# Kernel tuning notes

Hardware: AMD Instinct MI355X
Metric: run time of the kernel (lower is better)

Reference implementation:

```python
import jax, jax.numpy as jnp
import numpy as np

TOPK = 32

def softsign(x):
    return x / (1.0 + jnp.abs(x))

def setup_inputs() -> dict:
    key = jax.random.key(0)
    k1, k2, k3 = jax.random.split(key, 3)
    B, Q, S, D = 1, 4096, 32768, 256
    return {
        "query_val": jax.random.normal(k1, (B, Q, D), dtype=jnp.float32),
        "source_val": jax.random.normal(k2, (B, S, D), dtype=jnp.float32),
        "source_state": jax.random.normal(k3, (B, S), dtype=jnp.float32),
    }

def reference(query_val, source_val, source_state):
    # pairwise scores (dot-product similarity): [B, Q, S]
    scores = jnp.einsum("bqd,bsd->bqs", query_val, source_val)
    # global top-k over sources == streaming blockwise top-k merge in the original
    top_scores, top_idx = jax.lax.top_k(scores, TOPK)  # [B, Q, K]
    edges = softsign(top_scores)                        # edge_compress_fn
    # gather_state_by_indices: [B, Q, K]
    sel_state = jnp.take_along_axis(source_state[:, None, :], top_idx, axis=-1)
    # gather_val_by_indices: [B, Q, K, D]
    sel_val = jnp.take_along_axis(source_val[:, None, :, :], top_idx[..., None], axis=2)
    delta_state = jnp.sum(edges * sel_state, axis=-1)          # [B, Q]
    delta_val = jnp.sum(edges[..., None] * sel_val, axis=-2)   # [B, Q, D]
    return delta_state, delta_val
```

## Files before the change

kernel.cpp:

```cpp
#include <hip/hip_runtime.h>
#include <stdint.h>

typedef unsigned int u32;
typedef unsigned long long u64;
typedef unsigned short u16;
typedef unsigned char u8;

#define NQ 4096
#define NS 32768
#define ND 256
#define TOPK 32
#define CAP 256
#define CAP2 24
#define ZT 2.75f

#define QB 256
#define SB 32
#define NSLICE 32
#define SLICE (NS / NSLICE)
#define CH (SLICE / SB)

typedef __attribute__((ext_vector_type(8))) __bf16 bf16x8;
typedef __attribute__((ext_vector_type(4))) float f32x4;

#define QB_OFF   (NS * ND * 2)
#define TQ_OFF   (QB_OFF + NQ * ND * 2)
#define C8_OFF   (TQ_OFF + NQ * 4)
#define CD_OFF   (C8_OFF + NQ * NSLICE)

__device__ __forceinline__ u16 f2bf(float x) {
  u32 u = __float_as_uint(x);
  u32 r = u + 0x7FFFu + ((u >> 16) & 1u);
  return (u16)(r >> 16);
}

__global__ void k_prep_src(const float* __restrict__ src, uint4* __restrict__ dst) {
  int t = blockIdx.x * 256 + threadIdx.x;
  const float4* s4 = (const float4*)src + (size_t)t * 2;
  float4 a = s4[0], b = s4[1];
  uint4 o;
  o.x = (u32)f2bf(a.x) | ((u32)f2bf(a.y) << 16);
  o.y = (u32)f2bf(a.z) | ((u32)f2bf(a.w) << 16);
  o.z = (u32)f2bf(b.x) | ((u32)f2bf(b.y) << 16);
  o.w = (u32)f2bf(b.z) | ((u32)f2bf(b.w) << 16);
  dst[t] = o;
}

__global__ void k_prep_q(const float* __restrict__ qv, u16* __restrict__ qb,
                         float* __restrict__ tq) {
  int lane = threadIdx.x & 63, w = threadIdx.x >> 6;
  int q = blockIdx.x * 4 + w;
  float4 v = *((const float4*)(qv + (size_t)q * ND) + lane);
  uint2 p;
  p.x = (u32)f2bf(v.x) | ((u32)f2bf(v.y) << 16);
  p.y = (u32)f2bf(v.z) | ((u32)f2bf(v.w) << 16);
  *((uint2*)(qb + (size_t)q * ND) + lane) = p;
  float s = v.x * v.x + v.y * v.y + v.z * v.z + v.w * v.w;
  #pragma unroll
  for (int o = 1; o < 64; o <<= 1) s += __shfl_xor(s, o, 64);
  if (lane == 0) tq[q] = ZT * sqrtf(s);
}

__global__ __launch_bounds__(256, 2) void k_screen(
    const u16* __restrict__ qb, const u16* __restrict__ srcb,
    const float* __restrict__ tq, u8* __restrict__ cnt8, u32* __restrict__ cand2) {
  __shared__ __align__(16) u16 lds[2][SB * ND];
  __shared__ u32 bcnt[QB];
  const int tid  = threadIdx.x;
  const int lane = tid & 63;
  const int w    = tid >> 6;
  const int l15  = lane & 15, lhi = lane >> 4;

  const int id   = blockIdx.x;
  const int xcd  = id & 7;
  const int rank = id >> 3;
  const int by   = xcd * 4 + (rank >> 4);
  const int bx   = rank & 15;

  const int qbase = bx * QB + w * 64;
  const int sbase = by * SLICE;

  bcnt[tid] = 0u;

  bf16x8 afrag[4][8];
  float  thr[4][4];
  #pragma unroll
  for (int mt = 0; mt < 4; ++mt) {
    const u16* qp = qb + (size_t)(qbase + mt * 16 + l15) * ND;
    #pragma unroll
    for (int ks = 0; ks < 8; ++ks)
      afrag[mt][ks] = *((const bf16x8*)(qp + ks * 32 + lhi * 8));
    #pragma unroll
    for (int r = 0; r < 4; ++r) thr[mt][r] = tq[qbase + mt * 16 + lhi * 4 + r];
  }

  int goff[4];
  #pragma unroll
  for (int i = 0; i < 4; ++i) {
    int slot = i * 256 + tid;
    int row  = slot >> 5;
    int o    = (slot & 31) ^ (row & 7);
    goff[i]  = row * ND + o * 8;
  }

#define STAGE(b, c)                                                              \
  {                                                                              \
    const u16* sp_ = srcb + (size_t)(sbase + (c) * SB) * ND;                     \
    _Pragma("unroll")                                                            \
    for (int i_ = 0; i_ < 4; ++i_)                                               \
      __builtin_amdgcn_global_load_lds(                                          \
          (const __attribute__((address_space(1))) void*)(sp_ + goff[i_]),       \
          (__attribute__((address_space(3))) void*)(&lds[b][(i_ * 256 + tid) * 8]), \
          16, 0, 0);                                                             \
  }

#define COMPUTE(b, srow0)                                                        \
  {                                                                              \
    f32x4 acc[4][2];                                                             \
    _Pragma("unroll")                                                            \
    for (int mt = 0; mt < 4; ++mt)                                               \
      _Pragma("unroll")                                                          \
      for (int nt = 0; nt < 2; ++nt) acc[mt][nt] = (f32x4){0.f, 0.f, 0.f, 0.f};  \
    _Pragma("unroll")                                                            \
    for (int ks = 0; ks < 8; ++ks) {                                             \
      bf16x8 bfr[2];                                                             \
      _Pragma("unroll")                                                          \
      for (int nt = 0; nt < 2; ++nt) {                                           \
        int r_ = nt * 16 + l15;                                                  \
        int o_ = ks * 4 + lhi;                                                   \
        int slot_ = r_ * 32 + (o_ ^ (r_ & 7));                                   \
        bfr[nt] = *((const bf16x8*)(&lds[b][slot_ * 8]));                        \
      }                                                                          \
      _Pragma("unroll")                                                          \
      for (int mt = 0; mt < 4; ++mt)                                             \
        _Pragma("unroll")                                                        \
        for (int nt = 0; nt < 2; ++nt)                                           \
          acc[mt][nt] = __builtin_amdgcn_mfma_f32_16x16x32_bf16(                 \
              afrag[mt][ks], bfr[nt], acc[mt][nt], 0, 0, 0);                     \
    }                                                                            \
    _Pragma("unroll")                                                            \
    for (int mt = 0; mt < 4; ++mt)                                               \
      _Pragma("unroll")                                                          \
      for (int nt = 0; nt < 2; ++nt)                                             \
        _Pragma("unroll")                                                        \
        for (int r_ = 0; r_ < 4; ++r_) {                                         \
          float sc_ = acc[mt][nt][r_];                                           \
          if (sc_ > thr[mt][r_]) {                                               \
            int ql_ = w * 64 + mt * 16 + lhi * 4 + r_;                           \
            u32 off_ = atomicAdd(&bcnt[ql_], 1u);                                \
            if (off_ < CAP2)                                                     \
              cand2[(((size_t)(qbase + mt * 16 + lhi * 4 + r_)) * NSLICE + by) * CAP2 + off_] = \
                  ((u32)((srow0) + nt * 16 + l15) << 16) | (u32)f2bf(sc_);       \
          }                                                                      \
        }                                                                        \
  }

  STAGE(0, 0);
  __syncthreads();
  int cur = 0;
  for (int c = 0; c < CH - 1; ++c) {
    STAGE(cur ^ 1, c + 1);
    COMPUTE(cur, sbase + c * SB);
    __syncthreads();
    cur ^= 1;
  }
  COMPUTE(cur, sbase + (CH - 1) * SB);
#undef STAGE
#undef COMPUTE

  __syncthreads();
  {
    u32 c = bcnt[tid];
    cnt8[(size_t)by * NQ + bx * QB + tid] = (u8)(c < CAP2 ? c : CAP2);
  }
}

__global__ __launch_bounds__(256) void k_finish(
    const float* __restrict__ qval, const float* __restrict__ sval,
    const float* __restrict__ sstate, const u8* __restrict__ cnt8,
    const u32* __restrict__ cand2, float* __restrict__ out) {
  const int q = blockIdx.x;
  const int tid = threadIdx.x;
  const int lane = tid & 63, w = tid >> 6;
  __shared__ u16  scnt[NSLICE];
  __shared__ u16  soff[NSLICE];
  __shared__ u32  skey[CAP];
  __shared__ u32  sidxl[CAP];
  __shared__ float sexact[64];
  __shared__ u32  ssrc[64];
  __shared__ float fw[TOPK];
  __shared__ u32  fi[TOPK];

  if (tid < NSLICE) scnt[tid] = cnt8[(size_t)tid * NQ + q];
  skey[tid] = 0u;
  __syncthreads();
  if (tid == 0) {
    u32 a = 0;
    #pragma unroll
    for (int s = 0; s < NSLICE; ++s) { soff[s] = (u16)a; a += scnt[s]; }
  }
  __syncthreads();

  {
    int s = tid >> 3, j0 = tid & 7;
    #pragma unroll
    for (int rep = 0; rep < 3; ++rep) {
      int j = j0 + rep * 8;
      if (j < (int)scnt[s]) {
        int p = (int)soff[s] + j;
        if (p < CAP) {
          u32 ent = cand2[((size_t)q * NSLICE + s) * CAP2 + j];
          skey[p]  = ((ent & 0xFFFFu) << 8) | (u32)p;
          sidxl[p] = ent >> 16;
        }
      }
    }
  }
  __syncthreads();

  {
    u32 key = skey[tid];
    #pragma unroll
    for (int k = 2; k <= 256; k <<= 1) {
      #pragma unroll
      for (int j = k >> 1; j > 0; j >>= 1) {
        u32 o;
        if (j >= 64) {
          skey[tid] = key;
          __syncthreads();
          o = skey[tid ^ j];
          __syncthreads();
        } else {
          o = __shfl_xor(key, j, 64);
        }
        bool keepMax = ((tid & j) == 0) == ((tid & k) == 0);
        key = keepMax ? (key > o ? key : o) : (key > o ? o : key);
      }
    }
    skey[tid] = key;
  }
  __syncthreads();

  const int l16 = lane & 15, sub = lane >> 4;
  float4 qf[4];
  #pragma unroll
  for (int j = 0; j < 4; ++j)
    qf[j] = *((const float4*)(qval + (size_t)q * ND) + l16 * 4 + j);
  #pragma unroll
  for (int p = 0; p < 4; ++p) {
    int e = w * 16 + p * 4 + sub;
    u32 key = skey[e];
    u32 si = sidxl[key & 0xFFu];
    float dp = 0.f;
    if (key) {
      const float4* vp = (const float4*)(sval + (size_t)si * ND) + l16 * 4;
      #pragma unroll
      for (int j = 0; j < 4; ++j) {
        float4 v = vp[j];
        dp += qf[j].x * v.x + qf[j].y * v.y + qf[j].z * v.z + qf[j].w * v.w;
      }
    }
    #pragma unroll
    for (int o = 1; o < 16; o <<= 1) dp += __shfl_xor(dp, o, 64);
    if (l16 == 0) { sexact[e] = key ? dp : -3.0e38f; ssrc[e] = si; }
  }
  __syncthreads();

  if (w == 0) {
    float sc = sexact[lane];
    u32 si  = ssrc[lane];
    u32 kb  = __float_as_uint(sc);
    kb = kb ^ (u32)(((int)kb >> 31) | 0x80000000);
    u64 kk = ((u64)kb << 32) | (u32)(~si);
    #pragma unroll
    for (int k = 2; k <= 64; k <<= 1) {
      #pragma unroll
      for (int j = k >> 1; j > 0; j >>= 1) {
        u64 o = __shfl_xor(kk, j, 64);
        bool keepMax = (((lane & j) == 0) == ((lane & k) == 0));
        kk = keepMax ? (kk > o ? kk : o) : (kk > o ? o : kk);
      }
    }
    u32 si2 = ~((u32)kk);
    u32 kb2 = (u32)(kk >> 32);
    u32 fb  = (kb2 & 0x80000000u) ? (kb2 ^ 0x80000000u) : ~kb2;
    float s = __uint_as_float(fb);
    bool ok = (lane < TOPK) && (s > -1.0e38f);
    float edge = ok ? (s / (1.f + fabsf(s))) : 0.f;
    float contrib = ok ? edge * sstate[si2] : 0.f;
    if (lane < TOPK) { fw[lane] = edge; fi[lane] = ok ? si2 : 0u; }
    #pragma unroll
    for (int o = 1; o < 64; o <<= 1) contrib += __shfl_xor(contrib, o, 64);
    if (lane == 0) out[q] = contrib;
  }
  __syncthreads();

  float acc = 0.f;
  #pragma unroll 8
  for (int k = 0; k < TOPK; ++k)
    acc += fw[k] * sval[(size_t)fi[k] * ND + tid];
  out[NQ + (size_t)q * ND + tid] = acc;
}

extern "C" void kernel_launch(void* const* d_in, const int* in_sizes, int n_in,
                              void* d_out, int out_size, void* d_ws, size_t ws_size,
                              hipStream_t stream) {
  const float* qval   = (const float*)d_in[0];
  const float* sval   = (const float*)d_in[1];
  const float* sstate = (const float*)d_in[2];
  float* out = (float*)d_out;
  char*  ws  = (char*)d_ws;
  u16*   srcb  = (u16*)ws;
  u16*   qbuf  = (u16*)(ws + QB_OFF);
  float* tq    = (float*)(ws + TQ_OFF);
  u8*    cnt8  = (u8*)(ws + C8_OFF);
  u32*   cand2 = (u32*)(ws + CD_OFF);

  k_prep_src<<<(NS * ND / 8) / 256, 256, 0, stream>>>(sval, (uint4*)srcb);
  k_prep_q<<<NQ / 4, 256, 0, stream>>>(qval, qbuf, tq);
  k_screen<<<(NQ / QB) * NSLICE, 256, 0, stream>>>(qbuf, srcb, tq, cnt8, cand2);
  k_finish<<<NQ, 256, 0, stream>>>(qval, sval, sstate, cnt8, cand2, out);
}
```

Measured before the change: 151.7 us.

## Merge prep kernels, double-chunk screen pipeline, rescore only 48 candidates

Merges the two bf16 prep kernels into one launch so a kernel boundary disappears. The screen kernel now stages two source chunks per iteration into a 4-buffer LDS ring and computes both before one barrier, halving the barrier count at the cost of twice the LDS (64 KB), which may limit occupancy at 2 blocks/CU. The finish kernel rescores only the top 48 approximate candidates instead of 64, cutting fp32 gathers but raising the risk of missing a true top-32 entry when bf16 screening misorders scores.

```diff
diff --git a/kernel.cpp b/kernel.cpp
--- a/kernel.cpp
+++ b/kernel.cpp
@@ -34,37 +34,39 @@
   return (u16)(r >> 16);
 }
 
-__global__ void k_prep_src(const float* __restrict__ src, uint4* __restrict__ dst) {
-  int t = blockIdx.x * 256 + threadIdx.x;
-  const float4* s4 = (const float4*)src + (size_t)t * 2;
-  float4 a = s4[0], b = s4[1];
-  uint4 o;
-  o.x = (u32)f2bf(a.x) | ((u32)f2bf(a.y) << 16);
-  o.y = (u32)f2bf(a.z) | ((u32)f2bf(a.w) << 16);
-  o.z = (u32)f2bf(b.x) | ((u32)f2bf(b.y) << 16);
-  o.w = (u32)f2bf(b.z) | ((u32)f2bf(b.w) << 16);
-  dst[t] = o;
-}
-
-__global__ void k_prep_q(const float* __restrict__ qv, u16* __restrict__ qb,
-                         float* __restrict__ tq) {
-  int lane = threadIdx.x & 63, w = threadIdx.x >> 6;
-  int q = blockIdx.x * 4 + w;
-  float4 v = *((const float4*)(qv + (size_t)q * ND) + lane);
-  uint2 p;
-  p.x = (u32)f2bf(v.x) | ((u32)f2bf(v.y) << 16);
-  p.y = (u32)f2bf(v.z) | ((u32)f2bf(v.w) << 16);
-  *((uint2*)(qb + (size_t)q * ND) + lane) = p;
-  float s = v.x * v.x + v.y * v.y + v.z * v.z + v.w * v.w;
-  #pragma unroll
-  for (int o = 1; o < 64; o <<= 1) s += __shfl_xor(s, o, 64);
-  if (lane == 0) tq[q] = ZT * sqrtf(s);
+__global__ void k_prep(const float* __restrict__ src, uint4* __restrict__ dst,
+                       const float* __restrict__ qv, u16* __restrict__ qb,
+                       float* __restrict__ tq) {
+  const int b = blockIdx.x;
+  if (b < (NS * ND / 8) / 256) {
+    int t = b * 256 + threadIdx.x;
+    const float4* s4 = (const float4*)src + (size_t)t * 2;
+    float4 a = s4[0], c = s4[1];
+    uint4 o;
+    o.x = (u32)f2bf(a.x) | ((u32)f2bf(a.y) << 16);
+    o.y = (u32)f2bf(a.z) | ((u32)f2bf(a.w) << 16);
+    o.z = (u32)f2bf(c.x) | ((u32)f2bf(c.y) << 16);
+    o.w = (u32)f2bf(c.z) | ((u32)f2bf(c.w) << 16);
+    dst[t] = o;
+  } else {
+    int lane = threadIdx.x & 63, w = threadIdx.x >> 6;
+    int q = (b - (NS * ND / 8) / 256) * 4 + w;
+    float4 v = *((const float4*)(qv + (size_t)q * ND) + lane);
+    uint2 p;
+    p.x = (u32)f2bf(v.x) | ((u32)f2bf(v.y) << 16);
+    p.y = (u32)f2bf(v.z) | ((u32)f2bf(v.w) << 16);
+    *((uint2*)(qb + (size_t)q * ND) + lane) = p;
+    float s = v.x * v.x + v.y * v.y + v.z * v.z + v.w * v.w;
+    #pragma unroll
+    for (int o = 1; o < 64; o <<= 1) s += __shfl_xor(s, o, 64);
+    if (lane == 0) tq[q] = ZT * sqrtf(s);
+  }
 }
 
 __global__ __launch_bounds__(256, 2) void k_screen(
     const u16* __restrict__ qb, const u16* __restrict__ srcb,
     const float* __restrict__ tq, u8* __restrict__ cnt8, u32* __restrict__ cand2) {
-  __shared__ __align__(16) u16 lds[2][SB * ND];
+  __shared__ __align__(16) u16 lds[4][SB * ND];
   __shared__ u32 bcnt[QB];
   const int tid  = threadIdx.x;
   const int lane = tid & 63;
@@ -156,15 +158,20 @@
   }
 
   STAGE(0, 0);
+  STAGE(1, 1);
   __syncthreads();
   int cur = 0;
-  for (int c = 0; c < CH - 1; ++c) {
-    STAGE(cur ^ 1, c + 1);
+  for (int cc = 0; cc < CH / 2 - 1; ++cc) {
+    int c = 2 * cc;
+    STAGE(cur ^ 2, c + 2);
+    STAGE((cur ^ 2) | 1, c + 3);
     COMPUTE(cur, sbase + c * SB);
+    COMPUTE(cur | 1, sbase + (c + 1) * SB);
     __syncthreads();
-    cur ^= 1;
-  }
-  COMPUTE(cur, sbase + (CH - 1) * SB);
+    cur ^= 2;
+  }
+  COMPUTE(cur, sbase + (CH - 2) * SB);
+  COMPUTE(cur | 1, sbase + (CH - 1) * SB);
 #undef STAGE
 #undef COMPUTE
 
@@ -186,8 +193,8 @@
   __shared__ u16  soff[NSLICE];
   __shared__ u32  skey[CAP];
   __shared__ u32  sidxl[CAP];
-  __shared__ float sexact[64];
-  __shared__ u32  ssrc[64];
+  __shared__ float sexact[48];
+  __shared__ u32  ssrc[48];
   __shared__ float fw[TOPK];
   __shared__ u32  fi[TOPK];
 
@@ -247,8 +254,8 @@
   for (int j = 0; j < 4; ++j)
     qf[j] = *((const float4*)(qval + (size_t)q * ND) + l16 * 4 + j);
   #pragma unroll
-  for (int p = 0; p < 4; ++p) {
-    int e = w * 16 + p * 4 + sub;
+  for (int p = 0; p < 3; ++p) {
+    int e = w * 12 + p * 4 + sub;
     u32 key = skey[e];
     u32 si = sidxl[key & 0xFFu];
     float dp = 0.f;
@@ -267,8 +274,8 @@
   __syncthreads();
 
   if (w == 0) {
-    float sc = sexact[lane];
-    u32 si  = ssrc[lane];
+    float sc = (lane < 48) ? sexact[lane] : -3.0e38f;
+    u32 si  = (lane < 48) ? ssrc[lane] : 0u;
     u32 kb  = __float_as_uint(sc);
     kb = kb ^ (u32)(((int)kb >> 31) | 0x80000000);
     u64 kk = ((u64)kb << 32) | (u32)(~si);
@@ -316,8 +323,7 @@
   u8*    cnt8  = (u8*)(ws + C8_OFF);
   u32*   cand2 = (u32*)(ws + CD_OFF);
 
-  k_prep_src<<<(NS * ND / 8) / 256, 256, 0, stream>>>(sval, (uint4*)srcb);
-  k_prep_q<<<NQ / 4, 256, 0, stream>>>(qval, qbuf, tq);
+  k_prep<<<(NS * ND / 8) / 256 + NQ / 4, 256, 0, stream>>>(sval, (uint4*)srcb, qval, qbuf, tq);
   k_screen<<<(NQ / QB) * NSLICE, 256, 0, stream>>>(qbuf, srcb, tq, cnt8, cand2);
   k_finish<<<NQ, 256, 0, stream>>>(qval, sval, sstate, cnt8, cand2, out);
 }
```

Measured after the change: 139.9 us. 1.08x faster.
